# Kernel tuning notes

Measured on AMD Instinct MI355X. Metric: run time of the kernel, lower is better.

Reference implementation:

```python
import jax, jax.numpy as jnp
import numpy as np

B, T, F, U = 256, 1024, 64, 128  # batch, history_size, model_input_num, GRU units


def gru(x_seq, W, Uk, b, return_sequences):
    """Keras GRU (reset_after=True, recurrent_activation=sigmoid, activation=relu).
    x_seq: [B,T,F_in]; W: [F_in,3U]; Uk: [U,3U]; b: [2,3U] (input bias, recurrent bias).
    """
    b_i, b_r = b[0], b[1]
    xw = jnp.einsum('bti,iu->btu', x_seq, W) + b_i  # precompute input projection [B,T,3U]

    def step(h, xw_t):
        rec = h @ Uk + b_r                          # [B,3U]
        xz, xr, xh = jnp.split(xw_t, 3, axis=-1)
        rz, rr, rh = jnp.split(rec, 3, axis=-1)
        z = jax.nn.sigmoid(xz + rz)
        r = jax.nn.sigmoid(xr + rr)
        hh = jax.nn.relu(xh + r * rh)
        h_new = z * h + (1.0 - z) * hh
        return h_new, h_new

    h0 = jnp.zeros((x_seq.shape[0], Uk.shape[0]), dtype=x_seq.dtype)
    hT, hs = jax.lax.scan(step, h0, jnp.swapaxes(xw, 0, 1))  # scan over time
    if return_sequences:
        return jnp.swapaxes(hs, 0, 1), hT  # [B,T,U], [B,U]
    return hT, hT


def setup_inputs() -> dict:
    key = jax.random.key(0)
    ks = jax.random.split(key, 7)
    s_in1 = 1.0 / np.sqrt(F)
    s_rec = 1.0 / np.sqrt(U)
    return {
        'input_data': jax.random.normal(ks[0], (B, T, F), dtype=jnp.float32),
        'W1': jax.random.normal(ks[1], (F, 3 * U), dtype=jnp.float32) * s_in1,
        'U1': jax.random.normal(ks[2], (U, 3 * U), dtype=jnp.float32) * s_rec,
        'b1': jnp.zeros((2, 3 * U), dtype=jnp.float32),
        'W2': jax.random.normal(ks[3], (U, 3 * U), dtype=jnp.float32) * s_rec,
        'U2': jax.random.normal(ks[4], (U, 3 * U), dtype=jnp.float32) * s_rec,
        'b2': jnp.zeros((2, 3 * U), dtype=jnp.float32),
    }


def reference(input_data, W1, U1, b1, W2, U2, b2):
    seq1, state1 = gru(input_data, W1, U1, b1, return_sequences=True)
    x, state2 = gru(seq1, W2, U2, b2, return_sequences=False)
    return (x, state1, state2)
```

## Files before the change

### kernel.cpp

```cpp
#include <hip/hip_runtime.h>


#define TT 1024
#define FF 64
#define G3 384
#define XW_BYTES (1024ull * 384 * 256 * 2)

typedef __attribute__((ext_vector_type(8))) __bf16 bf16x8;
typedef __attribute__((ext_vector_type(4))) float f32x4;

#define MFMA(a, b, c) __builtin_amdgcn_mfma_f32_16x16x32_bf16((a), (b), (c), 0, 0, 0)

__device__ __forceinline__ float sigf(float x) {
    return __builtin_amdgcn_rcpf(1.0f + __expf(-x));
}

__device__ __forceinline__ f32x4 unpackv(uint2 v) {
    f32x4 o;
    o[0] = __uint_as_float(v.x << 16);
    o[1] = __uint_as_float(v.x & 0xFFFF0000u);
    o[2] = __uint_as_float(v.y << 16);
    o[3] = __uint_as_float(v.y & 0xFFFF0000u);
    return o;
}

__global__ void xw_prepass(
    const float* __restrict__ x, const float* __restrict__ W1,
    const float* __restrict__ b1, unsigned short* __restrict__ ws)
{
    const int tid = threadIdx.x, wave = tid >> 6, lane = tid & 63;
    const int quad = lane >> 4, lc = lane & 15;
    const int rb = blockIdx.x;
    const int t  = blockIdx.y * 4 + wave;

    const float* px = x + ((size_t)(rb * 16 + lc) * TT + t) * FF + quad * 8;
    f32x4 u0 = *(const f32x4*)px;
    f32x4 u1 = *(const f32x4*)(px + 4);
    f32x4 u2 = *(const f32x4*)(px + 32);
    f32x4 u3 = *(const f32x4*)(px + 36);
    bf16x8 xa0, xa1;
#pragma unroll
    for (int j = 0; j < 4; j++) {
        xa0[j] = (__bf16)u0[j]; xa0[j + 4] = (__bf16)u1[j];
        xa1[j] = (__bf16)u2[j]; xa1[j + 4] = (__bf16)u3[j];
    }

    uint2* wq = (uint2*)ws + ((size_t)t * 16 + rb) * 1536 + lane;
    for (int nt = 0; nt < 24; nt++) {
        const int g  = nt >> 3;
        const int cg = nt & 7;
        const int uc = cg * 16 + lc;
        float bi = b1[g * 128 + uc];
        if (g < 2) bi += b1[G3 + g * 128 + uc];
        bf16x8 w0, w1v;
#pragma unroll
        for (int j = 0; j < 8; j++) {
            w0[j]  = (__bf16)W1[(quad * 8 + j) * G3 + g * 128 + uc];
            w1v[j] = (__bf16)W1[(32 + quad * 8 + j) * G3 + g * 128 + uc];
        }
        f32x4 acc = {bi, bi, bi, bi};
        acc = MFMA(xa0, w0, acc);
        acc = MFMA(xa1, w1v, acc);
        unsigned int s0 = __builtin_bit_cast(unsigned short, (__bf16)acc[0]);
        unsigned int s1 = __builtin_bit_cast(unsigned short, (__bf16)acc[1]);
        unsigned int s2 = __builtin_bit_cast(unsigned short, (__bf16)acc[2]);
        unsigned int s3 = __builtin_bit_cast(unsigned short, (__bf16)acc[3]);
        uint2 st;
        st.x = s0 | (s1 << 16);
        st.y = s2 | (s3 << 16);
        wq[(size_t)(g * 8 + cg) * 64] = st;
    }
}

template <bool PRE>
__global__ __launch_bounds__(512, 2) void gru_persist(
    const float* __restrict__ x,  const float* __restrict__ W1,
    const float* __restrict__ U1, const float* __restrict__ b1,
    const float* __restrict__ W2, const float* __restrict__ U2,
    const float* __restrict__ b2, const unsigned short* __restrict__ xw,
    float* __restrict__ out)
{
    const int tid  = threadIdx.x;
    const int wave = tid >> 6;
    const int lane = tid & 63;
    const int quad = lane >> 4;
    const int lc   = lane & 15;
    const int row0 = blockIdx.x * 16;
    const int u    = wave * 16 + lc;

    __shared__ __align__(16) __bf16 h1s[2][16][136];
    __shared__ __align__(16) __bf16 h2s[2][16][136];
    for (int i = tid; i < 2 * 16 * 136; i += 512) {
        ((__bf16*)h1s)[i] = (__bf16)0.f;
        ((__bf16*)h2s)[i] = (__bf16)0.f;
    }

    bf16x8 U1B[3][4], W2B[3][4], U2B[3][4];
    bf16x8 W1B[3][2];
#pragma unroll
    for (int g = 0; g < 3; g++) {
#pragma unroll
        for (int kt = 0; kt < 4; kt++) {
            bf16x8 a, b, c;
#pragma unroll
            for (int j = 0; j < 8; j++) {
                int k = (kt * 32 + quad * 8 + j) * G3 + g * 128 + u;
                a[j] = (__bf16)U1[k];
                b[j] = (__bf16)W2[k];
                c[j] = (__bf16)U2[k];
            }
            U1B[g][kt] = a;
            W2B[g][kt] = b;
            U2B[g][kt] = c;
        }
        if constexpr (!PRE) {
#pragma unroll
            for (int kt = 0; kt < 2; kt++) {
                bf16x8 a;
#pragma unroll
                for (int j = 0; j < 8; j++)
                    a[j] = (__bf16)W1[(kt * 32 + quad * 8 + j) * G3 + g * 128 + u];
                W1B[g][kt] = a;
            }
        }
    }

    float c1z  = b1[u] + b1[G3 + u];
    float c1r  = b1[128 + u] + b1[G3 + 128 + u];
    float b1ih = b1[256 + u];
    float b1rh = b1[G3 + 256 + u];
    float c2z  = b2[u] + b2[G3 + u];
    float c2r  = b2[128 + u] + b2[G3 + 128 + u];
    float b2ih = b2[256 + u];
    float b2rh = b2[G3 + 256 + u];

    const uint2* xqb = (const uint2*)xw + (size_t)blockIdx.x * 1536
                       + wave * 64 + lane;
    uint2 xwv[3];
    if constexpr (PRE) {
#pragma unroll
        for (int g = 0; g < 3; g++)
            xwv[g] = xqb[(size_t)g * 512];
    }
    const float* xrow = x + (size_t)(row0 + lc) * (TT * FF) + quad * 8;

    float h1c[4] = {0, 0, 0, 0};
    float h2c[4] = {0, 0, 0, 0};

    __syncthreads();

#define STEP(T, PAR)                                                           \
    {                                                                          \
        bf16x8 A1[4];                                                          \
        _Pragma("unroll") for (int kt = 0; kt < 4; kt++)                       \
            A1[kt] = *(const bf16x8*)&h1s[PAR ^ 1][lc][kt * 32 + quad * 8];    \
        f32x4 z1, r1, rh1, xh1;                                                \
        if constexpr (PRE) {                                                   \
            z1  = unpackv(xwv[0]);                   \
            r1  = unpackv(xwv[1]);                                             \
            xh1 = unpackv(xwv[2]);                    \
            rh1 = (f32x4){b1rh, b1rh, b1rh, b1rh};                             \
            if ((T) + 1 < TT) {                                                \
                _Pragma("unroll") for (int g = 0; g < 3; g++)                  \
                    xwv[g] = xqb[(size_t)((T) + 1) * 24576 + g * 512];         \
            }                                                                  \
        } else {                                                               \
            const float* px = xrow + (size_t)(T) * FF;                         \
            f32x4 u0 = *(const f32x4*)px;                                      \
            f32x4 u1 = *(const f32x4*)(px + 4);                                \
            f32x4 u2 = *(const f32x4*)(px + 32);                               \
            f32x4 u3 = *(const f32x4*)(px + 36);                               \
            bf16x8 xa0, xa1;                                                   \
            _Pragma("unroll") for (int j = 0; j < 4; j++) {                    \
                xa0[j] = (__bf16)u0[j]; xa0[j + 4] = (__bf16)u1[j];            \
                xa1[j] = (__bf16)u2[j]; xa1[j + 4] = (__bf16)u3[j];            \
            }                                                                  \
            z1  = (f32x4){c1z, c1z, c1z, c1z};                                 \
            r1  = (f32x4){c1r, c1r, c1r, c1r};                                 \
            rh1 = (f32x4){b1rh, b1rh, b1rh, b1rh};                             \
            xh1 = (f32x4){b1ih, b1ih, b1ih, b1ih};                             \
            z1  = MFMA(xa0, W1B[0][0], z1);                                    \
            z1  = MFMA(xa1, W1B[0][1], z1);                                    \
            r1  = MFMA(xa0, W1B[1][0], r1);                                    \
            r1  = MFMA(xa1, W1B[1][1], r1);                                    \
            xh1 = MFMA(xa0, W1B[2][0], xh1);                                   \
            xh1 = MFMA(xa1, W1B[2][1], xh1);                                   \
        }                                                                      \
        _Pragma("unroll") for (int kt = 0; kt < 4; kt++) {                     \
            z1  = MFMA(A1[kt], U1B[0][kt], z1);                                \
            r1  = MFMA(A1[kt], U1B[1][kt], r1);                                \
            rh1 = MFMA(A1[kt], U1B[2][kt], rh1);                               \
        }                                                                      \
        _Pragma("unroll") for (int i = 0; i < 4; i++) {                        \
            float zf = sigf(z1[i]);                                            \
            float rf = sigf(r1[i]);                                            \
            float hh = fmaxf(xh1[i] + rf * rh1[i], 0.f);                       \
            h1c[i] = fmaf(zf, h1c[i] - hh, hh);                                \
            h1s[PAR][quad * 4 + i][u] = (__bf16)h1c[i];                        \
        }                                                                      \
        f32x4 z2  = (f32x4){c2z, c2z, c2z, c2z};                               \
        f32x4 r2  = (f32x4){c2r, c2r, c2r, c2r};                               \
        f32x4 xh2 = (f32x4){b2ih, b2ih, b2ih, b2ih};                           \
        f32x4 rh2 = (f32x4){b2rh, b2rh, b2rh, b2rh};                           \
        _Pragma("unroll") for (int kt = 0; kt < 4; kt++) {                     \
            z2  = MFMA(A1[kt], W2B[0][kt], z2);                                \
            r2  = MFMA(A1[kt], W2B[1][kt], r2);                                \
            xh2 = MFMA(A1[kt], W2B[2][kt], xh2);                               \
        }                                                                      \
        _Pragma("unroll") for (int kt = 0; kt < 4; kt++) {                     \
            bf16x8 A2 = *(const bf16x8*)&h2s[PAR][lc][kt * 32 + quad * 8];     \
            z2  = MFMA(A2, U2B[0][kt], z2);                                    \
            r2  = MFMA(A2, U2B[1][kt], r2);                                    \
            rh2 = MFMA(A2, U2B[2][kt], rh2);                                   \
        }                                                                      \
        if ((T) > 0) {                                                         \
            _Pragma("unroll") for (int i = 0; i < 4; i++) {                    \
                float zf = sigf(z2[i]);                                        \
                float rf = sigf(r2[i]);                                        \
                float hh = fmaxf(xh2[i] + rf * rh2[i], 0.f);                   \
                h2c[i] = fmaf(zf, h2c[i] - hh, hh);                            \
            }                                                                  \
        }                                                                      \
        _Pragma("unroll") for (int i = 0; i < 4; i++)                          \
            h2s[PAR ^ 1][quad * 4 + i][u] = (__bf16)h2c[i];                    \
        asm volatile("s_waitcnt lgkmcnt(0)\n\ts_barrier" ::: "memory");        \
    }

    for (int t = 0; t < TT; t += 2) {
        STEP(t, 0)
        STEP(t + 1, 1)
    }
#undef STEP

    {
        f32x4 z2  = (f32x4){c2z, c2z, c2z, c2z};
        f32x4 r2  = (f32x4){c2r, c2r, c2r, c2r};
        f32x4 xh2 = (f32x4){b2ih, b2ih, b2ih, b2ih};
        f32x4 rh2 = (f32x4){b2rh, b2rh, b2rh, b2rh};
#pragma unroll
        for (int kt = 0; kt < 4; kt++) {
            bf16x8 a1 = *(const bf16x8*)&h1s[1][lc][kt * 32 + quad * 8];
            bf16x8 a2 = *(const bf16x8*)&h2s[0][lc][kt * 32 + quad * 8];
            z2  = MFMA(a1, W2B[0][kt], z2);
            r2  = MFMA(a1, W2B[1][kt], r2);
            xh2 = MFMA(a1, W2B[2][kt], xh2);
            z2  = MFMA(a2, U2B[0][kt], z2);
            r2  = MFMA(a2, U2B[1][kt], r2);
            rh2 = MFMA(a2, U2B[2][kt], rh2);
        }
#pragma unroll
        for (int i = 0; i < 4; i++) {
            float zf = sigf(z2[i]);
            float rf = sigf(r2[i]);
            float hh = fmaxf(xh2[i] + rf * rh2[i], 0.f);
            h2c[i] = fmaf(zf, h2c[i] - hh, hh);
        }
    }

#pragma unroll
    for (int i = 0; i < 4; i++) {
        int r = row0 + quad * 4 + i;
        out[(size_t)r * 128 + u]         = h2c[i];
        out[32768 + (size_t)r * 128 + u] = h1c[i];
        out[65536 + (size_t)r * 128 + u] = h2c[i];
    }
}

extern "C" void kernel_launch(void* const* d_in, const int* in_sizes, int n_in,
                              void* d_out, int out_size, void* d_ws, size_t ws_size,
                              hipStream_t stream) {
    const float* x  = (const float*)d_in[0];
    const float* W1 = (const float*)d_in[1];
    const float* U1 = (const float*)d_in[2];
    const float* b1 = (const float*)d_in[3];
    const float* W2 = (const float*)d_in[4];
    const float* U2 = (const float*)d_in[5];
    const float* b2 = (const float*)d_in[6];
    float* out = (float*)d_out;

    if (ws_size >= XW_BYTES) {
        unsigned short* ws = (unsigned short*)d_ws;
        xw_prepass<<<dim3(16, 256), dim3(256), 0, stream>>>(x, W1, b1, ws);
        gru_persist<true><<<dim3(16), dim3(512), 0, stream>>>(
            x, W1, U1, b1, W2, U2, b2, ws, out);
    } else {
        gru_persist<false><<<dim3(16), dim3(512), 0, stream>>>(
            x, W1, U1, b1, W2, U2, b2, nullptr, out);
    }
}
```

Baseline: 1.247 ms.

## Stagger layer order across odd/even waves so MFMA and gate math overlap

Splits each time step into layer-1 and layer-2 phases and has odd waves run layer 2 before layer 1, while even waves keep the original order. Within a SIMD, one wave's gate math (exp/rcp on the VALU) can then overlap with another wave's MFMA chain instead of every wave contending for the same unit at once. It also seeds the MFMA accumulators directly from bias vectors held in registers and replaces the launch-bounds occupancy hint with amdgpu_waves_per_eu(2,2). The cost is two copies of the unrolled loop, which enlarges the code and may raise register pressure.

After: 1.408 ms. +13.0%, slower.

```diff
diff --git a/kernel.cpp b/kernel.cpp
--- a/kernel.cpp
+++ b/kernel.cpp
@@ -73,7 +73,9 @@
 }
 
 template <bool PRE>
-__global__ __launch_bounds__(512, 2) void gru_persist(
+__global__ __launch_bounds__(512)
+__attribute__((amdgpu_waves_per_eu(2, 2)))
+void gru_persist(
     const float* __restrict__ x,  const float* __restrict__ W1,
     const float* __restrict__ U1, const float* __restrict__ b1,
     const float* __restrict__ W2, const float* __restrict__ U2,
@@ -125,14 +127,22 @@
         }
     }
 
-    float c1z  = b1[u] + b1[G3 + u];
-    float c1r  = b1[128 + u] + b1[G3 + 128 + u];
-    float b1ih = b1[256 + u];
-    float b1rh = b1[G3 + 256 + u];
-    float c2z  = b2[u] + b2[G3 + u];
-    float c2r  = b2[128 + u] + b2[G3 + 128 + u];
-    float b2ih = b2[256 + u];
-    float b2rh = b2[G3 + 256 + u];
+    const float c1z  = b1[u] + b1[G3 + u];
+    const float c1r  = b1[128 + u] + b1[G3 + 128 + u];
+    const float b1ih = b1[256 + u];
+    const float b1rh = b1[G3 + 256 + u];
+    const float c2z  = b2[u] + b2[G3 + u];
+    const float c2r  = b2[128 + u] + b2[G3 + 128 + u];
+    const float b2ih = b2[256 + u];
+    const float b2rh = b2[G3 + 256 + u];
+    const f32x4 c1zq  = {c1z, c1z, c1z, c1z};
+    const f32x4 c1rq  = {c1r, c1r, c1r, c1r};
+    const f32x4 b1ihq = {b1ih, b1ih, b1ih, b1ih};
+    const f32x4 b1rhq = {b1rh, b1rh, b1rh, b1rh};
+    const f32x4 c2zq  = {c2z, c2z, c2z, c2z};
+    const f32x4 c2rq  = {c2r, c2r, c2r, c2r};
+    const f32x4 b2ihq = {b2ih, b2ih, b2ih, b2ih};
+    const f32x4 b2rhq = {b2rh, b2rh, b2rh, b2rh};
 
     const uint2* xqb = (const uint2*)xw + (size_t)blockIdx.x * 1536
                        + wave * 64 + lane;
@@ -149,94 +159,140 @@
 
     __syncthreads();
 
-#define STEP(T, PAR)                                                           \
+#define LOAD_A1(PAR)                                                           \
+    bf16x8 A1[4];                                                              \
+    _Pragma("unroll") for (int kt = 0; kt < 4; kt++)                           \
+        A1[kt] = *(const bf16x8*)&h1s[PAR ^ 1][lc][kt * 32 + quad * 8];
+
+#define L1_MFMA(T)                                                             \
+    f32x4 z1, r1, rh1, xh1;                                                    \
+    if constexpr (PRE) {                                                       \
+        z1  = unpackv(xwv[0]);                       \
+        r1  = unpackv(xwv[1]);                                                 \
+        xh1 = unpackv(xwv[2]);                        \
+        if ((T) + 1 < TT) {                                                    \
+            _Pragma("unroll") for (int g = 0; g < 3; g++)                      \
+                xwv[g] = xqb[(size_t)((T) + 1) * 24576 + g * 512];             \
+        }                                                                      \
+    } else {                                                                   \
+        const float* px = xrow + (size_t)(T) * FF;                             \
+        f32x4 u0 = *(const f32x4*)px;                                          \
+        f32x4 u1 = *(const f32x4*)(px + 4);                                    \
+        f32x4 u2 = *(const f32x4*)(px + 32);                                   \
+        f32x4 u3 = *(const f32x4*)(px + 36);                                   \
+        bf16x8 xa0, xa1;                                                       \
+        _Pragma("unroll") for (int j = 0; j < 4; j++) {                        \
+            xa0[j] = (__bf16)u0[j]; xa0[j + 4] = (__bf16)u1[j];                \
+            xa1[j] = (__bf16)u2[j]; xa1[j + 4] = (__bf16)u3[j];                \
+        }                                                                      \
+        z1  = MFMA(xa0, W1B[0][0], c1zq);                                      \
+        z1  = MFMA(xa1, W1B[0][1], z1);                                        \
+        r1  = MFMA(xa0, W1B[1][0], c1rq);                                      \
+        r1  = MFMA(xa1, W1B[1][1], r1);                                        \
+        xh1 = MFMA(xa0, W1B[2][0], b1ihq);                                     \
+        xh1 = MFMA(xa1, W1B[2][1], xh1);                                       \
+    }                                                                          \
+    rh1 = MFMA(A1[0], U1B[2][0], b1rhq);                                       \
+    z1  = MFMA(A1[0], U1B[0][0], z1);                                          \
+    r1  = MFMA(A1[0], U1B[1][0], r1);                                          \
+    _Pragma("unroll") for (int kt = 1; kt < 4; kt++) {                         \
+        z1  = MFMA(A1[kt], U1B[0][kt], z1);                                    \
+        r1  = MFMA(A1[kt], U1B[1][kt], r1);                                    \
+        rh1 = MFMA(A1[kt], U1B[2][kt], rh1);                                   \
+    }
+
+#define G1_GATES(PAR)                                                          \
+    _Pragma("unroll") for (int i = 0; i < 4; i++) {                            \
+        float zf = sigf(z1[i]);                                                \
+        float rf = sigf(r1[i]);                                                \
+        float hh = fmaxf(xh1[i] + rf * rh1[i], 0.f);                           \
+        h1c[i] = fmaf(zf, h1c[i] - hh, hh);                                    \
+        h1s[PAR][quad * 4 + i][u] = (__bf16)h1c[i];                            \
+    }
+
+#define L2_MFMA(PAR)                                                           \
+    f32x4 z2  = MFMA(A1[0], W2B[0][0], c2zq);                                  \
+    f32x4 r2  = MFMA(A1[0], W2B[1][0], c2rq);                                  \
+    f32x4 xh2 = MFMA(A1[0], W2B[2][0], b2ihq);                                 \
+    _Pragma("unroll") for (int kt = 1; kt < 4; kt++) {                         \
+        z2  = MFMA(A1[kt], W2B[0][kt], z2);                                    \
+        r2  = MFMA(A1[kt], W2B[1][kt], r2);                                    \
+        xh2 = MFMA(A1[kt], W2B[2][kt], xh2);                                   \
+    }                                                                          \
+    f32x4 rh2;                                                                 \
     {                                                                          \
-        bf16x8 A1[4];                                                          \
-        _Pragma("unroll") for (int kt = 0; kt < 4; kt++)                       \
-            A1[kt] = *(const bf16x8*)&h1s[PAR ^ 1][lc][kt * 32 + quad * 8];    \
-        f32x4 z1, r1, rh1, xh1;                                                \
-        if constexpr (PRE) {                                                   \
-            z1  = unpackv(xwv[0]);                   \
-            r1  = unpackv(xwv[1]);                                             \
-            xh1 = unpackv(xwv[2]);                    \
-            rh1 = (f32x4){b1rh, b1rh, b1rh, b1rh};                             \
-            if ((T) + 1 < TT) {                                                \
-                _Pragma("unroll") for (int g = 0; g < 3; g++)                  \
-                    xwv[g] = xqb[(size_t)((T) + 1) * 24576 + g * 512];         \
-            }                                                                  \
-        } else {                                                               \
-            const float* px = xrow + (size_t)(T) * FF;                         \
-            f32x4 u0 = *(const f32x4*)px;                                      \
-            f32x4 u1 = *(const f32x4*)(px + 4);                                \
-            f32x4 u2 = *(const f32x4*)(px + 32);                               \
-            f32x4 u3 = *(const f32x4*)(px + 36);                               \
-            bf16x8 xa0, xa1;                                                   \
-            _Pragma("unroll") for (int j = 0; j < 4; j++) {                    \
-                xa0[j] = (__bf16)u0[j]; xa0[j + 4] = (__bf16)u1[j];            \
-                xa1[j] = (__bf16)u2[j]; xa1[j + 4] = (__bf16)u3[j];            \
-            }                                                                  \
-            z1  = (f32x4){c1z, c1z, c1z, c1z};                                 \
-            r1  = (f32x4){c1r, c1r, c1r, c1r};                                 \
-            rh1 = (f32x4){b1rh, b1rh, b1rh, b1rh};                             \
-            xh1 = (f32x4){b1ih, b1ih, b1ih, b1ih};                             \
-            z1  = MFMA(xa0, W1B[0][0], z1);                                    \
-            z1  = MFMA(xa1, W1B[0][1], z1);                                    \
-            r1  = MFMA(xa0, W1B[1][0], r1);                                    \
-            r1  = MFMA(xa1, W1B[1][1], r1);                                    \
-            xh1 = MFMA(xa0, W1B[2][0], xh1);                                   \
-            xh1 = MFMA(xa1, W1B[2][1], xh1);                                   \
+        bf16x8 A2 = *(const bf16x8*)&h2s[PAR][lc][quad * 8];                   \
+        rh2 = MFMA(A2, U2B[2][0], b2rhq);                                      \
+        z2  = MFMA(A2, U2B[0][0], z2);                                         \
+        r2  = MFMA(A2, U2B[1][0], r2);                                         \
+    }                                                                          \
+    _Pragma("unroll") for (int kt = 1; kt < 4; kt++) {                         \
+        bf16x8 A2 = *(const bf16x8*)&h2s[PAR][lc][kt * 32 + quad * 8];         \
+        z2  = MFMA(A2, U2B[0][kt], z2);                                        \
+        r2  = MFMA(A2, U2B[1][kt], r2);                                        \
+        rh2 = MFMA(A2, U2B[2][kt], rh2);                                       \
+    }
+
+#define G2_GATES(T, PAR)                                                       \
+    if ((T) > 0) {                                                             \
+        _Pragma("unroll") for (int i = 0; i < 4; i++) {                        \
+            float zf = sigf(z2[i]);                                            \
+            float rf = sigf(r2[i]);                                            \
+            float hh = fmaxf(xh2[i] + rf * rh2[i], 0.f);                       \
+            h2c[i] = fmaf(zf, h2c[i] - hh, hh);                                \
         }                                                                      \
-        _Pragma("unroll") for (int kt = 0; kt < 4; kt++) {                     \
-            z1  = MFMA(A1[kt], U1B[0][kt], z1);                                \
-            r1  = MFMA(A1[kt], U1B[1][kt], r1);                                \
-            rh1 = MFMA(A1[kt], U1B[2][kt], rh1);                               \
-        }                                                                      \
-        _Pragma("unroll") for (int i = 0; i < 4; i++) {                        \
-            float zf = sigf(z1[i]);                                            \
-            float rf = sigf(r1[i]);                                            \
-            float hh = fmaxf(xh1[i] + rf * rh1[i], 0.f);                       \
-            h1c[i] = fmaf(zf, h1c[i] - hh, hh);                                \
-            h1s[PAR][quad * 4 + i][u] = (__bf16)h1c[i];                        \
-        }                                                                      \
-        f32x4 z2  = (f32x4){c2z, c2z, c2z, c2z};                               \
-        f32x4 r2  = (f32x4){c2r, c2r, c2r, c2r};                               \
-        f32x4 xh2 = (f32x4){b2ih, b2ih, b2ih, b2ih};                           \
-        f32x4 rh2 = (f32x4){b2rh, b2rh, b2rh, b2rh};                           \
-        _Pragma("unroll") for (int kt = 0; kt < 4; kt++) {                     \
-            z2  = MFMA(A1[kt], W2B[0][kt], z2);                                \
-            r2  = MFMA(A1[kt], W2B[1][kt], r2);                                \
-            xh2 = MFMA(A1[kt], W2B[2][kt], xh2);                               \
-        }                                                                      \
-        _Pragma("unroll") for (int kt = 0; kt < 4; kt++) {                     \
-            bf16x8 A2 = *(const bf16x8*)&h2s[PAR][lc][kt * 32 + quad * 8];     \
-            z2  = MFMA(A2, U2B[0][kt], z2);                                    \
-            r2  = MFMA(A2, U2B[1][kt], r2);                                    \
-            rh2 = MFMA(A2, U2B[2][kt], rh2);                                   \
-        }                                                                      \
-        if ((T) > 0) {                                                         \
-            _Pragma("unroll") for (int i = 0; i < 4; i++) {                    \
-                float zf = sigf(z2[i]);                                        \
-                float rf = sigf(r2[i]);                                        \
-                float hh = fmaxf(xh2[i] + rf * rh2[i], 0.f);                   \
-                h2c[i] = fmaf(zf, h2c[i] - hh, hh);                            \
-            }                                                                  \
-        }                                                                      \
-        _Pragma("unroll") for (int i = 0; i < 4; i++)                          \
-            h2s[PAR ^ 1][quad * 4 + i][u] = (__bf16)h2c[i];                    \
-        asm volatile("s_waitcnt lgkmcnt(0)\n\ts_barrier" ::: "memory");        \
-    }
-
-    for (int t = 0; t < TT; t += 2) {
-        STEP(t, 0)
-        STEP(t + 1, 1)
-    }
-#undef STEP
+    }                                                                          \
+    _Pragma("unroll") for (int i = 0; i < 4; i++)                              \
+        h2s[PAR ^ 1][quad * 4 + i][u] = (__bf16)h2c[i];
+
+#define END_BARRIER                                                            \
+    asm volatile("s_waitcnt lgkmcnt(0)\n\ts_barrier" ::: "memory");
+
+#define STEP_A(T, PAR)                                                         \
+    {                                                                          \
+        LOAD_A1(PAR)                                                           \
+        L1_MFMA(T)                                                             \
+        G1_GATES(PAR)                                                          \
+        L2_MFMA(PAR)                                                           \
+        G2_GATES(T, PAR)                                                       \
+        END_BARRIER                                                            \
+    }
+
+#define STEP_B(T, PAR)                                                         \
+    {                                                                          \
+        LOAD_A1(PAR)                                                           \
+        L2_MFMA(PAR)                                                           \
+        G2_GATES(T, PAR)                                                       \
+        L1_MFMA(T)                                                             \
+        G1_GATES(PAR)                                                          \
+        END_BARRIER                                                            \
+    }
+
+    if (wave & 1) {
+        for (int t = 0; t < TT; t += 2) {
+            STEP_B(t, 0)
+            STEP_B(t + 1, 1)
+        }
+    } else {
+        for (int t = 0; t < TT; t += 2) {
+            STEP_A(t, 0)
+            STEP_A(t + 1, 1)
+        }
+    }
+#undef STEP_A
+#undef STEP_B
+#undef LOAD_A1
+#undef L1_MFMA
+#undef G1_GATES
+#undef L2_MFMA
+#undef G2_GATES
+#undef END_BARRIER
 
     {
-        f32x4 z2  = (f32x4){c2z, c2z, c2z, c2z};
-        f32x4 r2  = (f32x4){c2r, c2r, c2r, c2r};
-        f32x4 xh2 = (f32x4){b2ih, b2ih, b2ih, b2ih};
-        f32x4 rh2 = (f32x4){b2rh, b2rh, b2rh, b2rh};
+        f32x4 z2  = c2zq;
+        f32x4 r2  = c2rq;
+        f32x4 xh2 = b2ihq;
+        f32x4 rh2 = b2rhq;
 #pragma unroll
         for (int kt = 0; kt < 4; kt++) {
             bf16x8 a1 = *(const bf16x8*)&h1s[1][lc][kt * 32 + quad * 8];
```

## Pipeline GRU layers across separate blocks with global-memory flag handoff

Applied to the files above, without the earlier changes.

Replaces the xw prepass plus a single persistent kernel running both layers with a layer-pipelined kernel. Producer blocks run layer 1, computing the input projection inline, and write each step's hidden state to a per-timestep global slot and set a release flag. Consumer blocks wait on those flags and run layer 2, so the two recurrences overlap and each block's serial chain per step is shorter. This adds a flag-clear launch, global round trips and spin-waits on the critical path, and relies on all 32 blocks being co-resident to avoid deadlock.

Measured after the change: 4.187 ms. 236% more time.

```diff
diff --git a/kernel.cpp b/kernel.cpp
--- a/kernel.cpp
+++ b/kernel.cpp
@@ -4,7 +4,10 @@
 #define TT 1024
 #define FF 64
 #define G3 384
-#define XW_BYTES (1024ull * 384 * 256 * 2)
+#define NB 16
+#define SLOT_BYTES 4096
+#define FLAG_BYTES ((size_t)NB * TT * 4)
+#define PIPE_WS_BYTES (FLAG_BYTES + (size_t)NB * TT * SLOT_BYTES)
 
 typedef __attribute__((ext_vector_type(8))) __bf16 bf16x8;
 typedef __attribute__((ext_vector_type(4))) float f32x4;
@@ -15,70 +18,264 @@
     return __builtin_amdgcn_rcpf(1.0f + __expf(-x));
 }
 
-__device__ __forceinline__ f32x4 unpackv(uint2 v) {
-    f32x4 o;
-    o[0] = __uint_as_float(v.x << 16);
-    o[1] = __uint_as_float(v.x & 0xFFFF0000u);
-    o[2] = __uint_as_float(v.y << 16);
-    o[3] = __uint_as_float(v.y & 0xFFFF0000u);
-    return o;
-}
-
-__global__ void xw_prepass(
-    const float* __restrict__ x, const float* __restrict__ W1,
-    const float* __restrict__ b1, unsigned short* __restrict__ ws)
-{
-    const int tid = threadIdx.x, wave = tid >> 6, lane = tid & 63;
-    const int quad = lane >> 4, lc = lane & 15;
-    const int rb = blockIdx.x;
-    const int t  = blockIdx.y * 4 + wave;
-
-    const float* px = x + ((size_t)(rb * 16 + lc) * TT + t) * FF + quad * 8;
-    f32x4 u0 = *(const f32x4*)px;
-    f32x4 u1 = *(const f32x4*)(px + 4);
-    f32x4 u2 = *(const f32x4*)(px + 32);
-    f32x4 u3 = *(const f32x4*)(px + 36);
-    bf16x8 xa0, xa1;
-#pragma unroll
-    for (int j = 0; j < 4; j++) {
-        xa0[j] = (__bf16)u0[j]; xa0[j + 4] = (__bf16)u1[j];
-        xa1[j] = (__bf16)u2[j]; xa1[j + 4] = (__bf16)u3[j];
-    }
-
-    uint2* wq = (uint2*)ws + ((size_t)t * 16 + rb) * 1536 + lane;
-    for (int nt = 0; nt < 24; nt++) {
-        const int g  = nt >> 3;
-        const int cg = nt & 7;
-        const int uc = cg * 16 + lc;
-        float bi = b1[g * 128 + uc];
-        if (g < 2) bi += b1[G3 + g * 128 + uc];
-        bf16x8 w0, w1v;
-#pragma unroll
-        for (int j = 0; j < 8; j++) {
-            w0[j]  = (__bf16)W1[(quad * 8 + j) * G3 + g * 128 + uc];
-            w1v[j] = (__bf16)W1[(32 + quad * 8 + j) * G3 + g * 128 + uc];
-        }
-        f32x4 acc = {bi, bi, bi, bi};
-        acc = MFMA(xa0, w0, acc);
-        acc = MFMA(xa1, w1v, acc);
-        unsigned int s0 = __builtin_bit_cast(unsigned short, (__bf16)acc[0]);
-        unsigned int s1 = __builtin_bit_cast(unsigned short, (__bf16)acc[1]);
-        unsigned int s2 = __builtin_bit_cast(unsigned short, (__bf16)acc[2]);
-        unsigned int s3 = __builtin_bit_cast(unsigned short, (__bf16)acc[3]);
-        uint2 st;
-        st.x = s0 | (s1 << 16);
-        st.y = s2 | (s3 << 16);
-        wq[(size_t)(g * 8 + cg) * 64] = st;
-    }
-}
-
-template <bool PRE>
-__global__ __launch_bounds__(512, 2) void gru_persist(
+__device__ __forceinline__ void wait_flag(const unsigned int* f) {
+    while (__hip_atomic_load(f, __ATOMIC_ACQUIRE, __HIP_MEMORY_SCOPE_AGENT) == 0u)
+        __builtin_amdgcn_s_sleep(1);
+}
+
+__global__ void flag_clear(unsigned int* f) {
+    f[blockIdx.x * 256 + threadIdx.x] = 0u;
+}
+
+__global__ __launch_bounds__(512)
+__attribute__((amdgpu_waves_per_eu(2, 2)))
+void gru_pipe(
     const float* __restrict__ x,  const float* __restrict__ W1,
     const float* __restrict__ U1, const float* __restrict__ b1,
     const float* __restrict__ W2, const float* __restrict__ U2,
-    const float* __restrict__ b2, const unsigned short* __restrict__ xw,
+    const float* __restrict__ b2, unsigned char* __restrict__ ws,
     float* __restrict__ out)
+{
+    const int tid  = threadIdx.x;
+    const int wave = tid >> 6;
+    const int lane = tid & 63;
+    const int quad = lane >> 4;
+    const int lc   = lane & 15;
+    const int u    = wave * 16 + lc;
+
+    __shared__ __align__(16) __bf16 hs[2][16][136];
+    for (int i = tid; i < 2 * 16 * 136; i += 512)
+        ((__bf16*)hs)[i] = (__bf16)0.f;
+
+    unsigned int* flags_all = (unsigned int*)ws;
+    unsigned char* slots_all = ws + FLAG_BYTES;
+
+    if (blockIdx.x < NB) {
+        const int bid  = blockIdx.x;
+        const int row0 = bid * 16;
+        unsigned int* flags = flags_all + (size_t)bid * TT;
+        unsigned char* slotb = slots_all + (size_t)bid * TT * SLOT_BYTES;
+
+        bf16x8 U1B[3][4], W1B[3][2];
+#pragma unroll
+        for (int g = 0; g < 3; g++) {
+#pragma unroll
+            for (int kt = 0; kt < 4; kt++) {
+                bf16x8 a;
+#pragma unroll
+                for (int j = 0; j < 8; j++)
+                    a[j] = (__bf16)U1[(kt * 32 + quad * 8 + j) * G3 + g * 128 + u];
+                U1B[g][kt] = a;
+            }
+#pragma unroll
+            for (int kt = 0; kt < 2; kt++) {
+                bf16x8 a;
+#pragma unroll
+                for (int j = 0; j < 8; j++)
+                    a[j] = (__bf16)W1[(kt * 32 + quad * 8 + j) * G3 + g * 128 + u];
+                W1B[g][kt] = a;
+            }
+        }
+        const float c1z  = b1[u] + b1[G3 + u];
+        const float c1r  = b1[128 + u] + b1[G3 + 128 + u];
+        const float b1ih = b1[256 + u];
+        const float b1rh = b1[G3 + 256 + u];
+        const f32x4 c1zq  = {c1z, c1z, c1z, c1z};
+        const f32x4 c1rq  = {c1r, c1r, c1r, c1r};
+        const f32x4 b1ihq = {b1ih, b1ih, b1ih, b1ih};
+        const f32x4 b1rhq = {b1rh, b1rh, b1rh, b1rh};
+
+        const float* xrow = x + (size_t)(row0 + lc) * (TT * FF) + quad * 8;
+        f32x4 xp[4];
+        xp[0] = *(const f32x4*)(xrow);
+        xp[1] = *(const f32x4*)(xrow + 4);
+        xp[2] = *(const f32x4*)(xrow + 32);
+        xp[3] = *(const f32x4*)(xrow + 36);
+
+        const int pr = tid >> 5;
+        const int pc = (tid & 31) * 4;
+
+        float h1c[4] = {0, 0, 0, 0};
+        __syncthreads();
+
+#define PSTEP(T, PAR)                                                          \
+    {                                                                          \
+        if ((T) > 0) {                     \
+            uint2 pv = *(const uint2*)&hs[PAR ^ 1][pr][pc];                    \
+            *(uint2*)(slotb + (size_t)((T) - 1) * SLOT_BYTES + pr * 256 +      \
+                      pc * 2) = pv;                                            \
+        }                                                                      \
+        bf16x8 xa0, xa1;                                                       \
+        _Pragma("unroll") for (int j = 0; j < 4; j++) {                        \
+            xa0[j] = (__bf16)xp[0][j]; xa0[j + 4] = (__bf16)xp[1][j];          \
+            xa1[j] = (__bf16)xp[2][j]; xa1[j + 4] = (__bf16)xp[3][j];          \
+        }                                                                      \
+        if ((T) + 1 < TT) {                               \
+            const float* px = xrow + (size_t)((T) + 1) * FF;                   \
+            xp[0] = *(const f32x4*)px;                                         \
+            xp[1] = *(const f32x4*)(px + 4);                                   \
+            xp[2] = *(const f32x4*)(px + 32);                                  \
+            xp[3] = *(const f32x4*)(px + 36);                                  \
+        }                                                                      \
+        bf16x8 A1[4];                                                          \
+        _Pragma("unroll") for (int kt = 0; kt < 4; kt++)                       \
+            A1[kt] = *(const bf16x8*)&hs[PAR ^ 1][lc][kt * 32 + quad * 8];     \
+        f32x4 z1  = MFMA(xa0, W1B[0][0], c1zq);                                \
+        z1        = MFMA(xa1, W1B[0][1], z1);                                  \
+        f32x4 r1  = MFMA(xa0, W1B[1][0], c1rq);                                \
+        r1        = MFMA(xa1, W1B[1][1], r1);                                  \
+        f32x4 xh1 = MFMA(xa0, W1B[2][0], b1ihq);                               \
+        xh1       = MFMA(xa1, W1B[2][1], xh1);                                 \
+        f32x4 rh1 = MFMA(A1[0], U1B[2][0], b1rhq);                             \
+        z1        = MFMA(A1[0], U1B[0][0], z1);                                \
+        r1        = MFMA(A1[0], U1B[1][0], r1);                                \
+        _Pragma("unroll") for (int kt = 1; kt < 4; kt++) {                     \
+            z1  = MFMA(A1[kt], U1B[0][kt], z1);                                \
+            r1  = MFMA(A1[kt], U1B[1][kt], r1);                                \
+            rh1 = MFMA(A1[kt], U1B[2][kt], rh1);                               \
+        }                                                                      \
+        _Pragma("unroll") for (int i = 0; i < 4; i++) {                        \
+            float zf = sigf(z1[i]);                                            \
+            float rf = sigf(r1[i]);                                            \
+            float hh = fmaxf(xh1[i] + rf * rh1[i], 0.f);                       \
+            h1c[i] = fmaf(zf, h1c[i] - hh, hh);                                \
+            hs[PAR][quad * 4 + i][u] = (__bf16)h1c[i];                         \
+        }                                                                      \
+        __threadfence();              \
+        asm volatile("s_waitcnt lgkmcnt(0)\n\ts_barrier" ::: "memory");        \
+        if ((T) > 0 && tid == 0)                                               \
+            __hip_atomic_store(flags + (T) - 1, 1u, __ATOMIC_RELEASE,          \
+                               __HIP_MEMORY_SCOPE_AGENT);                      \
+    }
+
+        for (int t = 0; t < TT; t += 2) {
+            PSTEP(t, 0)
+            PSTEP(t + 1, 1)
+        }
+#undef PSTEP
+
+        {
+            uint2 pv = *(const uint2*)&hs[1][pr][pc];
+            *(uint2*)(slotb + (size_t)(TT - 1) * SLOT_BYTES + pr * 256 + pc * 2) = pv;
+            __threadfence();
+            __syncthreads();
+            if (tid == 0)
+                __hip_atomic_store(flags + TT - 1, 1u, __ATOMIC_RELEASE,
+                                   __HIP_MEMORY_SCOPE_AGENT);
+        }
+#pragma unroll
+        for (int i = 0; i < 4; i++) {
+            int r = row0 + quad * 4 + i;
+            out[32768 + (size_t)r * 128 + u] = h1c[i];
+        }
+    } else {
+        const int bid  = blockIdx.x - NB;
+        const int row0 = bid * 16;
+        const unsigned int* flags = flags_all + (size_t)bid * TT;
+        const unsigned char* slotb = slots_all + (size_t)bid * TT * SLOT_BYTES;
+
+        bf16x8 W2B[3][4], U2B[3][4];
+#pragma unroll
+        for (int g = 0; g < 3; g++)
+#pragma unroll
+            for (int kt = 0; kt < 4; kt++) {
+                bf16x8 b, c;
+#pragma unroll
+                for (int j = 0; j < 8; j++) {
+                    int k = (kt * 32 + quad * 8 + j) * G3 + g * 128 + u;
+                    b[j] = (__bf16)W2[k];
+                    c[j] = (__bf16)U2[k];
+                }
+                W2B[g][kt] = b;
+                U2B[g][kt] = c;
+            }
+        const float c2z  = b2[u] + b2[G3 + u];
+        const float c2r  = b2[128 + u] + b2[G3 + 128 + u];
+        const float b2ih = b2[256 + u];
+        const float b2rh = b2[G3 + 256 + u];
+        const f32x4 c2zq  = {c2z, c2z, c2z, c2z};
+        const f32x4 c2rq  = {c2r, c2r, c2r, c2r};
+        const f32x4 b2ihq = {b2ih, b2ih, b2ih, b2ih};
+        const f32x4 b2rhq = {b2rh, b2rh, b2rh, b2rh};
+
+        const unsigned char* abase = slotb + lc * 256 + quad * 16;
+        float h2c[4] = {0, 0, 0, 0};
+        __syncthreads();
+
+        wait_flag(flags);
+        bf16x8 Aa0, Aa1, Aa2, Aa3, Ab0, Ab1, Ab2, Ab3;
+        Aa0 = *(const bf16x8*)(abase);
+        Aa1 = *(const bf16x8*)(abase + 64);
+        Aa2 = *(const bf16x8*)(abase + 128);
+        Aa3 = *(const bf16x8*)(abase + 192);
+
+#define CSTEP(T, PAR, C0, C1, C2, C3, N0, N1, N2, N3)                          \
+    {                                                                          \
+        if ((T) + 1 < TT) {               \
+            wait_flag(flags + (T) + 1);                                        \
+            const unsigned char* sp = abase + (size_t)((T) + 1) * SLOT_BYTES;  \
+            N0 = *(const bf16x8*)(sp);                                         \
+            N1 = *(const bf16x8*)(sp + 64);                                    \
+            N2 = *(const bf16x8*)(sp + 128);                                   \
+            N3 = *(const bf16x8*)(sp + 192);                                   \
+        }                                                                      \
+        f32x4 z2  = MFMA(C0, W2B[0][0], c2zq);                                 \
+        f32x4 r2  = MFMA(C0, W2B[1][0], c2rq);                                 \
+        f32x4 xh2 = MFMA(C0, W2B[2][0], b2ihq);                                \
+        z2  = MFMA(C1, W2B[0][1], z2);                                         \
+        r2  = MFMA(C1, W2B[1][1], r2);                                         \
+        xh2 = MFMA(C1, W2B[2][1], xh2);                                        \
+        z2  = MFMA(C2, W2B[0][2], z2);                                         \
+        r2  = MFMA(C2, W2B[1][2], r2);                                         \
+        xh2 = MFMA(C2, W2B[2][2], xh2);                                        \
+        z2  = MFMA(C3, W2B[0][3], z2);                                         \
+        r2  = MFMA(C3, W2B[1][3], r2);                                         \
+        xh2 = MFMA(C3, W2B[2][3], xh2);                                        \
+        f32x4 rh2;                                                             \
+        {                                                                      \
+            bf16x8 A2 = *(const bf16x8*)&hs[PAR ^ 1][lc][quad * 8];            \
+            rh2 = MFMA(A2, U2B[2][0], b2rhq);                                  \
+            z2  = MFMA(A2, U2B[0][0], z2);                                     \
+            r2  = MFMA(A2, U2B[1][0], r2);                                     \
+        }                                                                      \
+        _Pragma("unroll") for (int kt = 1; kt < 4; kt++) {                     \
+            bf16x8 A2 = *(const bf16x8*)&hs[PAR ^ 1][lc][kt * 32 + quad * 8];  \
+            z2  = MFMA(A2, U2B[0][kt], z2);                                    \
+            r2  = MFMA(A2, U2B[1][kt], r2);                                    \
+            rh2 = MFMA(A2, U2B[2][kt], rh2);                                   \
+        }                                                                      \
+        _Pragma("unroll") for (int i = 0; i < 4; i++) {                        \
+            float zf = sigf(z2[i]);                                            \
+            float rf = sigf(r2[i]);                                            \
+            float hh = fmaxf(xh2[i] + rf * rh2[i], 0.f);                       \
+            h2c[i] = fmaf(zf, h2c[i] - hh, hh);                                \
+            hs[PAR][quad * 4 + i][u] = (__bf16)h2c[i];                         \
+        }                                                                      \
+        asm volatile("s_waitcnt lgkmcnt(0)\n\ts_barrier" ::: "memory");        \
+    }
+
+        for (int t = 0; t < TT; t += 2) {
+            CSTEP(t, 0, Aa0, Aa1, Aa2, Aa3, Ab0, Ab1, Ab2, Ab3)
+            CSTEP(t + 1, 1, Ab0, Ab1, Ab2, Ab3, Aa0, Aa1, Aa2, Aa3)
+        }
+#undef CSTEP
+
+#pragma unroll
+        for (int i = 0; i < 4; i++) {
+            int r = row0 + quad * 4 + i;
+            out[(size_t)r * 128 + u]         = h2c[i];
+            out[65536 + (size_t)r * 128 + u] = h2c[i];
+        }
+    }
+}
+
+__global__ __launch_bounds__(512)
+__attribute__((amdgpu_waves_per_eu(2, 2)))
+void gru_mono(
+    const float* __restrict__ x,  const float* __restrict__ W1,
+    const float* __restrict__ U1, const float* __restrict__ b1,
+    const float* __restrict__ W2, const float* __restrict__ U2,
+    const float* __restrict__ b2, float* __restrict__ out)
 {
     const int tid  = threadIdx.x;
     const int wave = tid >> 6;
@@ -95,8 +292,7 @@
         ((__bf16*)h2s)[i] = (__bf16)0.f;
     }
 
-    bf16x8 U1B[3][4], W2B[3][4], U2B[3][4];
-    bf16x8 W1B[3][2];
+    bf16x8 U1B[3][4], W2B[3][4], U2B[3][4], W1B[3][2];
 #pragma unroll
     for (int g = 0; g < 3; g++) {
 #pragma unroll
@@ -109,84 +305,65 @@
                 b[j] = (__bf16)W2[k];
                 c[j] = (__bf16)U2[k];
             }
-            U1B[g][kt] = a;
-            W2B[g][kt] = b;
-            U2B[g][kt] = c;
-        }
-        if constexpr (!PRE) {
-#pragma unroll
-            for (int kt = 0; kt < 2; kt++) {
-                bf16x8 a;
-#pragma unroll
-                for (int j = 0; j < 8; j++)
-                    a[j] = (__bf16)W1[(kt * 32 + quad * 8 + j) * G3 + g * 128 + u];
-                W1B[g][kt] = a;
-            }
-        }
-    }
-
-    float c1z  = b1[u] + b1[G3 + u];
-    float c1r  = b1[128 + u] + b1[G3 + 128 + u];
-    float b1ih = b1[256 + u];
-    float b1rh = b1[G3 + 256 + u];
-    float c2z  = b2[u] + b2[G3 + u];
-    float c2r  = b2[128 + u] + b2[G3 + 128 + u];
-    float b2ih = b2[256 + u];
-    float b2rh = b2[G3 + 256 + u];
-
-    const uint2* xqb = (const uint2*)xw + (size_t)blockIdx.x * 1536
-                       + wave * 64 + lane;
-    uint2 xwv[3];
-    if constexpr (PRE) {
-#pragma unroll
-        for (int g = 0; g < 3; g++)
-            xwv[g] = xqb[(size_t)g * 512];
-    }
+            U1B[g][kt] = a; W2B[g][kt] = b; U2B[g][kt] = c;
+        }
+#pragma unroll
+        for (int kt = 0; kt < 2; kt++) {
+            bf16x8 a;
+#pragma unroll
+            for (int j = 0; j < 8; j++)
+                a[j] = (__bf16)W1[(kt * 32 + quad * 8 + j) * G3 + g * 128 + u];
+            W1B[g][kt] = a;
+        }
+    }
+
+    const float c1z  = b1[u] + b1[G3 + u];
+    const float c1r  = b1[128 + u] + b1[G3 + 128 + u];
+    const float b1ih = b1[256 + u];
+    const float b1rh = b1[G3 + 256 + u];
+    const float c2z  = b2[u] + b2[G3 + u];
+    const float c2r  = b2[128 + u] + b2[G3 + 128 + u];
+    const float b2ih = b2[256 + u];
+    const float b2rh = b2[G3 + 256 + u];
+    const f32x4 c1zq  = {c1z, c1z, c1z, c1z};
+    const f32x4 c1rq  = {c1r, c1r, c1r, c1r};
+    const f32x4 b1ihq = {b1ih, b1ih, b1ih, b1ih};
+    const f32x4 b1rhq = {b1rh, b1rh, b1rh, b1rh};
+    const f32x4 c2zq  = {c2z, c2z, c2z, c2z};
+    const f32x4 c2rq  = {c2r, c2r, c2r, c2r};
+    const f32x4 b2ihq = {b2ih, b2ih, b2ih, b2ih};
+    const f32x4 b2rhq = {b2rh, b2rh, b2rh, b2rh};
+
     const float* xrow = x + (size_t)(row0 + lc) * (TT * FF) + quad * 8;
-
     float h1c[4] = {0, 0, 0, 0};
     float h2c[4] = {0, 0, 0, 0};
-
     __syncthreads();
 
-#define STEP(T, PAR)                                                           \
+#define MSTEP(T, PAR)                                                          \
     {                                                                          \
         bf16x8 A1[4];                                                          \
         _Pragma("unroll") for (int kt = 0; kt < 4; kt++)                       \
             A1[kt] = *(const bf16x8*)&h1s[PAR ^ 1][lc][kt * 32 + quad * 8];    \
-        f32x4 z1, r1, rh1, xh1;                                                \
-        if constexpr (PRE) {                                                   \
-            z1  = unpackv(xwv[0]);                   \
-            r1  = unpackv(xwv[1]);                                             \
-            xh1 = unpackv(xwv[2]);                    \
-            rh1 = (f32x4){b1rh, b1rh, b1rh, b1rh};                             \
-            if ((T) + 1 < TT) {                                                \
-                _Pragma("unroll") for (int g = 0; g < 3; g++)                  \
-                    xwv[g] = xqb[(size_t)((T) + 1) * 24576 + g * 512];         \
-            }                                                                  \
-        } else {                                                               \
-            const float* px = xrow + (size_t)(T) * FF;                         \
-            f32x4 u0 = *(const f32x4*)px;                                      \
-            f32x4 u1 = *(const f32x4*)(px + 4);                                \
-            f32x4 u2 = *(const f32x4*)(px + 32);                               \
-            f32x4 u3 = *(const f32x4*)(px + 36);                               \
-            bf16x8 xa0, xa1;                                                   \
-            _Pragma("unroll") for (int j = 0; j < 4; j++) {                    \
-                xa0[j] = (__bf16)u0[j]; xa0[j + 4] = (__bf16)u1[j];            \
-                xa1[j] = (__bf16)u2[j]; xa1[j + 4] = (__bf16)u3[j];            \
-            }                                                                  \
-            z1  = (f32x4){c1z, c1z, c1z, c1z};                                 \
-            r1  = (f32x4){c1r, c1r, c1r, c1r};                                 \
-            rh1 = (f32x4){b1rh, b1rh, b1rh, b1rh};                             \
-            xh1 = (f32x4){b1ih, b1ih, b1ih, b1ih};                             \
-            z1  = MFMA(xa0, W1B[0][0], z1);                                    \
-            z1  = MFMA(xa1, W1B[0][1], z1);                                    \
-            r1  = MFMA(xa0, W1B[1][0], r1);                                    \
-            r1  = MFMA(xa1, W1B[1][1], r1);                                    \
-            xh1 = MFMA(xa0, W1B[2][0], xh1);                                   \
-            xh1 = MFMA(xa1, W1B[2][1], xh1);                                   \
-        }                                                                      \
-        _Pragma("unroll") for (int kt = 0; kt < 4; kt++) {                     \
+        const float* px = xrow + (size_t)(T) * FF;                             \
+        f32x4 u0 = *(const f32x4*)px;                                          \
+        f32x4 u1 = *(const f32x4*)(px + 4);                                    \
+        f32x4 u2 = *(const f32x4*)(px + 32);                                   \
+        f32x4 u3 = *(const f32x4*)(px + 36);                                   \
+        bf16x8 xa0, xa1;                                                       \
+        _Pragma("unroll") for (int j = 0; j < 4; j++) {                        \
+            xa0[j] = (__bf16)u0[j]; xa0[j + 4] = (__bf16)u1[j];                \
+            xa1[j] = (__bf16)u2[j]; xa1[j + 4] = (__bf16)u3[j];                \
+        }                                                                      \
+        f32x4 z1  = MFMA(xa0, W1B[0][0], c1zq);                                \
+        z1        = MFMA(xa1, W1B[0][1], z1);                                  \
+        f32x4 r1  = MFMA(xa0, W1B[1][0], c1rq);                                \
+        r1        = MFMA(xa1, W1B[1][1], r1);                                  \
+        f32x4 xh1 = MFMA(xa0, W1B[2][0], b1ihq);                               \
+        xh1       = MFMA(xa1, W1B[2][1], xh1);                                 \
+        f32x4 rh1 = MFMA(A1[0], U1B[2][0], b1rhq);                             \
+        z1        = MFMA(A1[0], U1B[0][0], z1);                                \
+        r1        = MFMA(A1[0], U1B[1][0], r1);                                \
+        _Pragma("unroll") for (int kt = 1; kt < 4; kt++) {                     \
             z1  = MFMA(A1[kt], U1B[0][kt], z1);                                \
             r1  = MFMA(A1[kt], U1B[1][kt], r1);                                \
             rh1 = MFMA(A1[kt], U1B[2][kt], rh1);                               \
@@ -198,16 +375,22 @@
             h1c[i] = fmaf(zf, h1c[i] - hh, hh);                                \
             h1s[PAR][quad * 4 + i][u] = (__bf16)h1c[i];                        \
         }                                                                      \
-        f32x4 z2  = (f32x4){c2z, c2z, c2z, c2z};                               \
-        f32x4 r2  = (f32x4){c2r, c2r, c2r, c2r};                               \
-        f32x4 xh2 = (f32x4){b2ih, b2ih, b2ih, b2ih};                           \
-        f32x4 rh2 = (f32x4){b2rh, b2rh, b2rh, b2rh};                           \
-        _Pragma("unroll") for (int kt = 0; kt < 4; kt++) {                     \
+        f32x4 z2  = MFMA(A1[0], W2B[0][0], c2zq);                              \
+        f32x4 r2  = MFMA(A1[0], W2B[1][0], c2rq);                              \
+        f32x4 xh2 = MFMA(A1[0], W2B[2][0], b2ihq);                             \
+        _Pragma("unroll") for (int kt = 1; kt < 4; kt++) {                     \
             z2  = MFMA(A1[kt], W2B[0][kt], z2);                                \
             r2  = MFMA(A1[kt], W2B[1][kt], r2);                                \
             xh2 = MFMA(A1[kt], W2B[2][kt], xh2);                               \
         }                                                                      \
-        _Pragma("unroll") for (int kt = 0; kt < 4; kt++) {                     \
+        f32x4 rh2;                                                             \
+        {                                                                      \
+            bf16x8 A2 = *(const bf16x8*)&h2s[PAR][lc][quad * 8];               \
+            rh2 = MFMA(A2, U2B[2][0], b2rhq);                                  \
+            z2  = MFMA(A2, U2B[0][0], z2);                                     \
+            r2  = MFMA(A2, U2B[1][0], r2);                                     \
+        }                                                                      \
+        _Pragma("unroll") for (int kt = 1; kt < 4; kt++) {                     \
             bf16x8 A2 = *(const bf16x8*)&h2s[PAR][lc][kt * 32 + quad * 8];     \
             z2  = MFMA(A2, U2B[0][kt], z2);                                    \
             r2  = MFMA(A2, U2B[1][kt], r2);                                    \
@@ -227,16 +410,13 @@
     }
 
     for (int t = 0; t < TT; t += 2) {
-        STEP(t, 0)
-        STEP(t + 1, 1)
-    }
-#undef STEP
+        MSTEP(t, 0)
+        MSTEP(t + 1, 1)
+    }
+#undef MSTEP
 
     {
-        f32x4 z2  = (f32x4){c2z, c2z, c2z, c2z};
-        f32x4 r2  = (f32x4){c2r, c2r, c2r, c2r};
-        f32x4 xh2 = (f32x4){b2ih, b2ih, b2ih, b2ih};
-        f32x4 rh2 = (f32x4){b2rh, b2rh, b2rh, b2rh};
+        f32x4 z2 = c2zq, r2 = c2rq, xh2 = b2ihq, rh2 = b2rhq;
 #pragma unroll
         for (int kt = 0; kt < 4; kt++) {
             bf16x8 a1 = *(const bf16x8*)&h1s[1][lc][kt * 32 + quad * 8];
@@ -278,13 +458,13 @@
     const float* b2 = (const float*)d_in[6];
     float* out = (float*)d_out;
 
-    if (ws_size >= XW_BYTES) {
-        unsigned short* ws = (unsigned short*)d_ws;
-        xw_prepass<<<dim3(16, 256), dim3(256), 0, stream>>>(x, W1, b1, ws);
-        gru_persist<true><<<dim3(16), dim3(512), 0, stream>>>(
+    if (ws_size >= PIPE_WS_BYTES) {
+        unsigned char* ws = (unsigned char*)d_ws;
+        flag_clear<<<dim3(NB * TT / 256), dim3(256), 0, stream>>>((unsigned int*)ws);
+        gru_pipe<<<dim3(2 * NB), dim3(512), 0, stream>>>(
             x, W1, U1, b1, W2, U2, b2, ws, out);
     } else {
-        gru_persist<false><<<dim3(16), dim3(512), 0, stream>>>(
-            x, W1, U1, b1, W2, U2, b2, nullptr, out);
-    }
-}
+        gru_mono<<<dim3(NB), dim3(512), 0, stream>>>(
+            x, W1, U1, b1, W2, U2, b2, out);
+    }
+}
```
